# Kernel tuning notes

Hardware: AMD Instinct MI355X
Metric: run time of the kernel (lower is better)

Reference implementation:

```python
import jax, jax.numpy as jnp
import numpy as np

SIZE = 512
ATTN = 64      # per-head attention_size
OUT = 64       # per-head output_size
HEADS = 8

def setup_inputs() -> dict:
    key = jax.random.key(0)
    ks = jax.random.split(key, 7)
    s = 0.02
    return {
        "x":  jax.random.normal(ks[0], (4, 2048, SIZE), dtype=jnp.float32),
        "Wq": jax.random.normal(ks[1], (SIZE, ATTN * HEADS), dtype=jnp.float32) * s,
        "bq": jax.random.normal(ks[2], (ATTN * HEADS,), dtype=jnp.float32) * s,
        "Wk": jax.random.normal(ks[3], (SIZE, ATTN), dtype=jnp.float32) * s,  # shared key, no bias
        "Wv": jax.random.normal(ks[4], (SIZE, OUT * HEADS), dtype=jnp.float32) * s,
        "bv": jax.random.normal(ks[5], (OUT * HEADS,), dtype=jnp.float32) * s,
    }

def reference(x, Wq, bq, Wk, Wv, bv):
    B, S, _ = x.shape
    q = (x @ Wq + bq).reshape(B, S, HEADS, ATTN)   # (B,S,H,A)
    k = x @ Wk                                      # (B,S,A) shared across heads
    v = (x @ Wv + bv).reshape(B, S, HEADS, OUT)     # (B,S,H,O)
    # NOTE: original divides by sqrt(seq_len), not sqrt(head_dim)
    scale = 1.0 / np.sqrt(S).astype(np.float32)
    scores = jnp.einsum("bqha,bka->bhqk", q, k) * scale  # (B,H,S,S)
    causal = jnp.tril(jnp.ones((S, S), dtype=bool))
    scores = jnp.where(causal, scores, -jnp.inf)
    attn = jax.nn.softmax(scores, axis=-1)
    out = jnp.einsum("bhqk,bkho->bqho", attn, v)    # (B,S,H,O)
    return out.reshape(B, S, HEADS * OUT)
```

## Files before the change

kernel.cpp:

```cpp
#include <hip/hip_runtime.h>
#include <math.h>


typedef _Float16 half8 __attribute__((ext_vector_type(8)));
typedef _Float16 half4 __attribute__((ext_vector_type(4)));
typedef float float4v __attribute__((ext_vector_type(4)));
typedef unsigned int u32;

#define SCL2E 0.031885926f

__device__ inline float4v mfma16(half8 a, half8 b, float4v c) {
    return __builtin_amdgcn_mfma_f32_16x16x32_f16(a, b, c, 0, 0, 0);
}
__device__ inline void load16(const _Float16* g, _Float16* l) {
    __builtin_amdgcn_global_load_lds((const __attribute__((address_space(1))) u32*)g,
                                     (__attribute__((address_space(3))) u32*)l, 16, 0, 0);
}

__global__ __launch_bounds__(256) void prep(
    const float* __restrict__ x, const float* __restrict__ Wq,
    const float* __restrict__ Wk, const float* __restrict__ Wv,
    _Float16* __restrict__ xh, _Float16* __restrict__ wqt,
    _Float16* __restrict__ wkt, _Float16* __restrict__ wvt) {
    const int bid = blockIdx.x;
    if (bid < 2048) {
        size_t base = (size_t)bid * 2048 + (size_t)threadIdx.x * 8;
        const float4* xp = (const float4*)(x + base);
        float4 f0 = xp[0], f1 = xp[1];
        half8 h = {(_Float16)f0.x, (_Float16)f0.y, (_Float16)f0.z, (_Float16)f0.w,
                   (_Float16)f1.x, (_Float16)f1.y, (_Float16)f1.z, (_Float16)f1.w};
        *(half8*)(xh + base) = h;
    } else {
        int r = bid - 2048;
        const float* W; _Float16* WT; int N, bx, by;
        if (r < 256)      { W = Wq; WT = wqt; N = 512; bx = r & 15; by = r >> 4; }
        else if (r < 288) { r -= 256; W = Wk; WT = wkt; N = 64;  bx = r & 1;  by = r >> 1; }
        else              { r -= 288; W = Wv; WT = wvt; N = 512; bx = r & 15; by = r >> 4; }
        __shared__ float T[32][33];
        const int tx = threadIdx.x & 31, ty = threadIdx.x >> 5;
        const int n0 = bx * 32, k0 = by * 32;
#pragma unroll
        for (int i = 0; i < 4; ++i)
            T[ty + 8 * i][tx] = W[(size_t)(k0 + ty + 8 * i) * N + n0 + tx];
        __syncthreads();
#pragma unroll
        for (int i = 0; i < 4; ++i)
            WT[(size_t)(n0 + ty + 8 * i) * 512 + k0 + tx] = (_Float16)T[tx][ty + 8 * i];
    }
}

__global__ __launch_bounds__(256) void qkv_gemm(
    const _Float16* __restrict__ xh,
    const _Float16* __restrict__ wqt, const _Float16* __restrict__ wkt,
    const _Float16* __restrict__ wvt,
    const float* __restrict__ bq, const float* __restrict__ bv,
    _Float16* __restrict__ q_ws, _Float16* __restrict__ kt_ws, _Float16* __restrict__ vt_ws) {
    __shared__ __align__(16) _Float16 Xs[2][8192];
    __shared__ __align__(16) _Float16 Ws[2][4096];

    const int m0 = blockIdx.x * 128;
    const int nt = blockIdx.y;
    const _Float16* WT;
    const float* bias;
    if (nt < 8)       { WT = wqt + (size_t)nt * 64 * 512; bias = bq + nt * 64; }
    else if (nt == 8) { WT = wkt;                          bias = nullptr; }
    else              { WT = wvt + (size_t)(nt - 9) * 64 * 512; bias = bv + (nt - 9) * 64; }

    const int tid = threadIdx.x;
    const int w = tid >> 6, lane = tid & 63, quad = lane >> 4, cl = lane & 15;
    const int lrow = lane >> 3;
    const int lgc = (lane & 7) ^ lrow;
    const _Float16* xg = xh + (size_t)(m0 + lrow) * 512 + lgc * 8;
    const _Float16* wg = WT + (size_t)lrow * 512 + lgc * 8;

    const int g0 = (quad ^ (cl & 7)) << 3;
    const int g1 = ((quad ^ 4) ^ (cl & 7)) << 3;

    float4v acc[2][4] = {};

#pragma unroll
    for (int c = 0; c < 4; ++c) {
        int cc = w * 4 + c;
        load16(xg + (size_t)cc * 8 * 512, Xs[0] + cc * 512);
    }
#pragma unroll
    for (int c = 0; c < 2; ++c) {
        int cc = w * 2 + c;
        load16(wg + (size_t)cc * 8 * 512, Ws[0] + cc * 512);
    }

    for (int ki = 0; ki < 8; ++ki) {
        const int cb = ki & 1, nb = cb ^ 1;
        __syncthreads();
        if (ki < 7) {
            const int kk = (ki + 1) * 64;
#pragma unroll
            for (int c = 0; c < 4; ++c) {
                int cc = w * 4 + c;
                load16(xg + (size_t)cc * 8 * 512 + kk, Xs[nb] + cc * 512);
            }
#pragma unroll
            for (int c = 0; c < 2; ++c) {
                int cc = w * 2 + c;
                load16(wg + (size_t)cc * 8 * 512 + kk, Ws[nb] + cc * 512);
            }
        }
#pragma unroll
        for (int c = 0; c < 2; ++c) {
            const int g = c ? g1 : g0;
#pragma unroll
            for (int s = 0; s < 2; ++s) {
                half8 a = *(const half8*)(Xs[cb] + (w * 32 + s * 16 + cl) * 64 + g);
#pragma unroll
                for (int j = 0; j < 4; ++j) {
                    half8 b = *(const half8*)(Ws[cb] + (j * 16 + cl) * 64 + g);
                    acc[s][j] = mfma16(a, b, acc[s][j]);
                }
            }
        }
    }

    if (nt < 8) {
#pragma unroll
        for (int s = 0; s < 2; ++s)
#pragma unroll
            for (int j = 0; j < 4; ++j)
#pragma unroll
                for (int r = 0; r < 4; ++r) {
                    int lr = w * 32 + s * 16 + quad * 4 + r;
                    int col = j * 16 + cl;
                    q_ws[(size_t)(m0 + lr) * 512 + nt * 64 + col] =
                        (_Float16)((acc[s][j][r] + bias[col]) * SCL2E);
                }
    } else if (nt == 8) {
#pragma unroll
        for (int s = 0; s < 2; ++s)
#pragma unroll
            for (int j = 0; j < 4; ++j)
#pragma unroll
                for (int r = 0; r < 4; ++r) {
                    int grow = m0 + w * 32 + s * 16 + quad * 4 + r;
                    int b = grow >> 11, t = (grow >> 6) & 31, row = grow & 63;
                    int col = j * 16 + cl;
                    kt_ws[((size_t)(b * 32 + t) << 12) + row * 64 +
                          (((col >> 3) ^ (row & 7)) << 3) + (col & 7)] = (_Float16)acc[s][j][r];
                }
    } else {
        const int h = nt - 9;
#pragma unroll
        for (int s = 0; s < 2; ++s)
#pragma unroll
            for (int j = 0; j < 4; ++j)
#pragma unroll
                for (int r = 0; r < 4; ++r) {
                    int grow = m0 + w * 32 + s * 16 + quad * 4 + r;
                    int b = grow >> 11, t = (grow >> 6) & 31, row = grow & 63;
                    int o = j * 16 + cl;
                    int kap = ((row & 15) << 2) + (row >> 4);
                    vt_ws[(((size_t)(b * 8 + h) * 32 + t) << 12) + o * 64 +
                          (((kap >> 3) ^ (o & 7)) << 3) + (kap & 7)] =
                        (_Float16)(acc[s][j][r] + bias[o]);
                }
    }
}

__global__ __launch_bounds__(512, 2) void attn(
    const _Float16* __restrict__ q_ws, const _Float16* __restrict__ kt_ws,
    const _Float16* __restrict__ vt_ws, float* __restrict__ out) {
    __shared__ __align__(16) _Float16 Ks[2][2][4096];
    __shared__ __align__(16) _Float16 VTs[2][2][4096];
    __shared__ __align__(16) _Float16 Ps[8][1024];

    const int bh = blockIdx.x, b = bh >> 3, h = bh & 7;
    const int p = 31 - blockIdx.y;
    const int q0 = p * 64;
    const int nmax = (p + 2) >> 1;

    const int bS = b * 2048;
    const int tid = threadIdx.x;
    const int w = tid >> 6, lane = tid & 63, quad = lane >> 4, cl = lane & 15;
    const int g = w >> 2, wl = w & 3;
    const int tbase = g ? nmax : 0;
    const int nit = g ? (p + 1 - nmax) : nmax;

    const _Float16* kbase = kt_ws + ((size_t)(b * 32) << 12);
    const _Float16* vbase = vt_ws + ((size_t)((b * 8 + h) * 32) << 12);

    const int g0 = (quad ^ (cl & 7)) << 3;
    const int g1 = ((quad ^ 4) ^ (cl & 7)) << 3;
    const int so0 = wl * 1024 + lane * 8;

    const _Float16* qbase = q_ws + (size_t)(bS + q0 + wl * 16 + cl) * 512 + h * 64;
    half8 qa0 = *(const half8*)(qbase + quad * 8);
    half8 qa1 = *(const half8*)(qbase + 32 + quad * 8);

    float4v oacc[4] = {};
    float l_run[4] = {0.f, 0.f, 0.f, 0.f};

    if (nit > 0) {
        const _Float16* kt = kbase + ((size_t)tbase << 12);
        const _Float16* vt = vbase + ((size_t)tbase << 12);
        load16(kt + so0,       &Ks[g][0][wl * 1024]);
        load16(kt + so0 + 512, &Ks[g][0][wl * 1024 + 512]);
        load16(vt + so0,       &VTs[g][0][wl * 1024]);
        load16(vt + so0 + 512, &VTs[g][0][wl * 1024 + 512]);
    }

    for (int t = 0; t < nmax; ++t) {
        const int cb = t & 1, nb = cb ^ 1;
        __syncthreads();
        const int tg = tbase + t;
        if (t + 1 < nit) {
            const _Float16* kt = kbase + ((size_t)(tg + 1) << 12);
            const _Float16* vt = vbase + ((size_t)(tg + 1) << 12);
            load16(kt + so0,       &Ks[g][nb][wl * 1024]);
            load16(kt + so0 + 512, &Ks[g][nb][wl * 1024 + 512]);
            load16(vt + so0,       &VTs[g][nb][wl * 1024]);
            load16(vt + so0 + 512, &VTs[g][nb][wl * 1024 + 512]);
        }
        if (t < nit) {
            if (tg != p) {
                float4v sfr[4];
#pragma unroll
                for (int j = 0; j < 4; ++j) {
                    const _Float16* kr = &Ks[g][cb][(j * 16 + cl) * 64];
                    half8 b0 = *(const half8*)(kr + g0);
                    half8 b1 = *(const half8*)(kr + g1);
                    float4v a_ = {0.f, 0.f, 0.f, 0.f};
                    a_ = mfma16(qa0, b0, a_);
                    a_ = mfma16(qa1, b1, a_);
                    sfr[j] = a_;
                }
#pragma unroll
                for (int r = 0; r < 4; ++r) {
                    float p0 = exp2f(sfr[0][r]), p1 = exp2f(sfr[1][r]);
                    float p2 = exp2f(sfr[2][r]), p3 = exp2f(sfr[3][r]);
                    l_run[r] += (p0 + p1) + (p2 + p3);
                    int rr = quad * 4 + r;
                    half4 ph = {(_Float16)p0, (_Float16)p1, (_Float16)p2, (_Float16)p3};
                    *(half4*)&Ps[w][rr * 64 + ((((cl >> 1) ^ (rr & 7)) << 3) | ((cl & 1) << 2))] = ph;
                }
            } else {
                const int jmax = wl;
                float4v sfr[4];
#pragma unroll
                for (int j = 0; j < 4; ++j) {
                    if (j <= jmax) {
                        const _Float16* kr = &Ks[g][cb][(j * 16 + cl) * 64];
                        half8 b0 = *(const half8*)(kr + g0);
                        half8 b1 = *(const half8*)(kr + g1);
                        float4v a_ = {0.f, 0.f, 0.f, 0.f};
                        a_ = mfma16(qa0, b0, a_);
                        a_ = mfma16(qa1, b1, a_);
                        sfr[j] = a_;
                    }
                }
#pragma unroll
                for (int r = 0; r < 4; ++r) {
                    float pj[4];
#pragma unroll
                    for (int j = 0; j < 4; ++j) {
                        bool live = (j < jmax) || (j == jmax && cl <= quad * 4 + r);
                        pj[j] = live ? exp2f(sfr[j][r]) : 0.f;
                    }
                    l_run[r] += (pj[0] + pj[1]) + (pj[2] + pj[3]);
                    int rr = quad * 4 + r;
                    half4 ph = {(_Float16)pj[0], (_Float16)pj[1], (_Float16)pj[2], (_Float16)pj[3]};
                    *(half4*)&Ps[w][rr * 64 + ((((cl >> 1) ^ (rr & 7)) << 3) | ((cl & 1) << 2))] = ph;
                }
            }
            const _Float16* PB = &Ps[w][cl * 64];
            half8 pa0 = *(const half8*)(PB + g0);
            half8 pa1 = *(const half8*)(PB + g1);
#pragma unroll
            for (int jo = 0; jo < 4; ++jo) {
                const _Float16* vr = &VTs[g][cb][(jo * 16 + cl) * 64];
                half8 v0 = *(const half8*)(vr + g0);
                half8 v1 = *(const half8*)(vr + g1);
                oacc[jo] = mfma16(pa0, v0, oacc[jo]);
                oacc[jo] = mfma16(pa1, v1, oacc[jo]);
            }
        }
    }

    __syncthreads();
    float* Obuf = (float*)&Ks[1][0][0];
    float* Lbuf = (float*)&Ps[4][0];
    if (g == 1) {
#pragma unroll
        for (int jo = 0; jo < 4; ++jo)
#pragma unroll
            for (int r = 0; r < 4; ++r) {
                int row = wl * 16 + quad * 4 + r;
                Obuf[row * 64 + jo * 16 + cl] = oacc[jo][r];
            }
#pragma unroll
        for (int r = 0; r < 4; ++r) {
            int row = wl * 16 + quad * 4 + r;
            Lbuf[row * 16 + cl] = l_run[r];
        }
    }
    __syncthreads();
    if (g == 0) {
#pragma unroll
        for (int r = 0; r < 4; ++r) {
            int row = wl * 16 + quad * 4 + r;
            float l = l_run[r] + Lbuf[row * 16 + cl];
            l += __shfl_xor(l, 1);
            l += __shfl_xor(l, 2);
            l += __shfl_xor(l, 4);
            l += __shfl_xor(l, 8);
            float inv = 1.0f / l;
            float* op = out + (size_t)(bS + q0 + row) * 512 + h * 64 + cl;
            op[0]  = (oacc[0][r] + Obuf[row * 64 +      cl]) * inv;
            op[16] = (oacc[1][r] + Obuf[row * 64 + 16 + cl]) * inv;
            op[32] = (oacc[2][r] + Obuf[row * 64 + 32 + cl]) * inv;
            op[48] = (oacc[3][r] + Obuf[row * 64 + 48 + cl]) * inv;
        }
    }
}

extern "C" void kernel_launch(void* const* d_in, const int* in_sizes, int n_in,
                              void* d_out, int out_size, void* d_ws, size_t ws_size,
                              hipStream_t stream) {
    const float* x  = (const float*)d_in[0];
    const float* Wq = (const float*)d_in[1];
    const float* bq = (const float*)d_in[2];
    const float* Wk = (const float*)d_in[3];
    const float* Wv = (const float*)d_in[4];
    const float* bv = (const float*)d_in[5];
    float* out = (float*)d_out;

    char* ws = (char*)d_ws;
    _Float16* q_ws  = (_Float16*)(ws);
    _Float16* kt_ws = (_Float16*)(ws + 8388608);
    _Float16* vt_ws = (_Float16*)(ws + 9437184);
    _Float16* wqt   = (_Float16*)(ws + 17825792);
    _Float16* wkt   = (_Float16*)(ws + 18350080);
    _Float16* wvt   = (_Float16*)(ws + 18415616);
    _Float16* xh    = (_Float16*)(ws + 18939904);

    prep<<<dim3(2592), dim3(256), 0, stream>>>(x, Wq, Wk, Wv, xh, wqt, wkt, wvt);

    qkv_gemm<<<dim3(64, 17), dim3(256), 0, stream>>>(
        xh, wqt, wkt, wvt, bq, bv, q_ws, kt_ws, vt_ws);

    attn<<<dim3(32, 32), dim3(512), 0, stream>>>(q_ws, kt_ws, vt_ws, out);
}
```

Baseline: 142.8 us.

## Skew group-1 warps to overlap P·V of previous tile with next QK

Refactors the tile loop into staging, QK/softmax and PV lambdas. The second warp group now runs a skewed software pipeline: it does the P·V of the previous tile, then stages the next K tile and the current V tile, then computes QK for the current tile, with a final P·V after the loop. The goal is to stagger the MFMA and LDS phases between the two warp groups and hide load latency. The V for the current tile is loaded within the same iteration without a barrier before its use, and the Lbuf location moves, so there are correctness and timing risks around sync and async LDS loads.

Result: faster. 137.9 us (median of 3 runs) (-3.4%).

```diff
diff --git a/kernel.cpp b/kernel.cpp
--- a/kernel.cpp
+++ b/kernel.cpp
@@ -197,33 +197,49 @@
     float4v oacc[4] = {};
     float l_run[4] = {0.f, 0.f, 0.f, 0.f};
 
-    if (nit > 0) {
-        const _Float16* kt = kbase + ((size_t)tbase << 12);
-        const _Float16* vt = vbase + ((size_t)tbase << 12);
-        load16(kt + so0,       &Ks[g][0][wl * 1024]);
-        load16(kt + so0 + 512, &Ks[g][0][wl * 1024 + 512]);
-        load16(vt + so0,       &VTs[g][0][wl * 1024]);
-        load16(vt + so0 + 512, &VTs[g][0][wl * 1024 + 512]);
-    }
-
-    for (int t = 0; t < nmax; ++t) {
-        const int cb = t & 1, nb = cb ^ 1;
-        __syncthreads();
-        const int tg = tbase + t;
-        if (t + 1 < nit) {
-            const _Float16* kt = kbase + ((size_t)(tg + 1) << 12);
-            const _Float16* vt = vbase + ((size_t)(tg + 1) << 12);
-            load16(kt + so0,       &Ks[g][nb][wl * 1024]);
-            load16(kt + so0 + 512, &Ks[g][nb][wl * 1024 + 512]);
-            load16(vt + so0,       &VTs[g][nb][wl * 1024]);
-            load16(vt + so0 + 512, &VTs[g][nb][wl * 1024 + 512]);
-        }
-        if (t < nit) {
-            if (tg != p) {
-                float4v sfr[4];
-#pragma unroll
-                for (int j = 0; j < 4; ++j) {
-                    const _Float16* kr = &Ks[g][cb][(j * 16 + cl) * 64];
+    _Float16* KsG = &Ks[g][0][0];
+    _Float16* VsG = &VTs[g][0][0];
+
+    auto stageK = [&](int tile, int buf) {
+        const _Float16* kt = kbase + ((size_t)tile << 12);
+        load16(kt + so0,       KsG + buf * 4096 + wl * 1024);
+        load16(kt + so0 + 512, KsG + buf * 4096 + wl * 1024 + 512);
+    };
+    auto stageV = [&](int tile, int buf) {
+        const _Float16* vt = vbase + ((size_t)tile << 12);
+        load16(vt + so0,       VsG + buf * 4096 + wl * 1024);
+        load16(vt + so0 + 512, VsG + buf * 4096 + wl * 1024 + 512);
+    };
+    auto qk_sm = [&](int tg, int buf) {
+        const _Float16* KB = KsG + buf * 4096;
+        if (tg != p) {
+            float4v sfr[4];
+#pragma unroll
+            for (int j = 0; j < 4; ++j) {
+                const _Float16* kr = KB + (j * 16 + cl) * 64;
+                half8 b0 = *(const half8*)(kr + g0);
+                half8 b1 = *(const half8*)(kr + g1);
+                float4v a_ = {0.f, 0.f, 0.f, 0.f};
+                a_ = mfma16(qa0, b0, a_);
+                a_ = mfma16(qa1, b1, a_);
+                sfr[j] = a_;
+            }
+#pragma unroll
+            for (int r = 0; r < 4; ++r) {
+                float p0 = exp2f(sfr[0][r]), p1 = exp2f(sfr[1][r]);
+                float p2 = exp2f(sfr[2][r]), p3 = exp2f(sfr[3][r]);
+                l_run[r] += (p0 + p1) + (p2 + p3);
+                int rr = quad * 4 + r;
+                half4 ph = {(_Float16)p0, (_Float16)p1, (_Float16)p2, (_Float16)p3};
+                *(half4*)&Ps[w][rr * 64 + ((((cl >> 1) ^ (rr & 7)) << 3) | ((cl & 1) << 2))] = ph;
+            }
+        } else {
+            const int jmax = wl;
+            float4v sfr[4];
+#pragma unroll
+            for (int j = 0; j < 4; ++j) {
+                if (j <= jmax) {
+                    const _Float16* kr = KB + (j * 16 + cl) * 64;
                     half8 b0 = *(const half8*)(kr + g0);
                     half8 b1 = *(const half8*)(kr + g1);
                     float4v a_ = {0.f, 0.f, 0.f, 0.f};
@@ -231,61 +247,65 @@
                     a_ = mfma16(qa1, b1, a_);
                     sfr[j] = a_;
                 }
-#pragma unroll
-                for (int r = 0; r < 4; ++r) {
-                    float p0 = exp2f(sfr[0][r]), p1 = exp2f(sfr[1][r]);
-                    float p2 = exp2f(sfr[2][r]), p3 = exp2f(sfr[3][r]);
-                    l_run[r] += (p0 + p1) + (p2 + p3);
-                    int rr = quad * 4 + r;
-                    half4 ph = {(_Float16)p0, (_Float16)p1, (_Float16)p2, (_Float16)p3};
-                    *(half4*)&Ps[w][rr * 64 + ((((cl >> 1) ^ (rr & 7)) << 3) | ((cl & 1) << 2))] = ph;
-                }
-            } else {
-                const int jmax = wl;
-                float4v sfr[4];
+            }
+#pragma unroll
+            for (int r = 0; r < 4; ++r) {
+                float pj[4];
 #pragma unroll
                 for (int j = 0; j < 4; ++j) {
-                    if (j <= jmax) {
-                        const _Float16* kr = &Ks[g][cb][(j * 16 + cl) * 64];
-                        half8 b0 = *(const half8*)(kr + g0);
-                        half8 b1 = *(const half8*)(kr + g1);
-                        float4v a_ = {0.f, 0.f, 0.f, 0.f};
-                        a_ = mfma16(qa0, b0, a_);
-                        a_ = mfma16(qa1, b1, a_);
-                        sfr[j] = a_;
-                    }
-                }
-#pragma unroll
-                for (int r = 0; r < 4; ++r) {
-                    float pj[4];
-#pragma unroll
-                    for (int j = 0; j < 4; ++j) {
-                        bool live = (j < jmax) || (j == jmax && cl <= quad * 4 + r);
-                        pj[j] = live ? exp2f(sfr[j][r]) : 0.f;
-                    }
-                    l_run[r] += (pj[0] + pj[1]) + (pj[2] + pj[3]);
-                    int rr = quad * 4 + r;
-                    half4 ph = {(_Float16)pj[0], (_Float16)pj[1], (_Float16)pj[2], (_Float16)pj[3]};
-                    *(half4*)&Ps[w][rr * 64 + ((((cl >> 1) ^ (rr & 7)) << 3) | ((cl & 1) << 2))] = ph;
-                }
-            }
-            const _Float16* PB = &Ps[w][cl * 64];
-            half8 pa0 = *(const half8*)(PB + g0);
-            half8 pa1 = *(const half8*)(PB + g1);
-#pragma unroll
-            for (int jo = 0; jo < 4; ++jo) {
-                const _Float16* vr = &VTs[g][cb][(jo * 16 + cl) * 64];
-                half8 v0 = *(const half8*)(vr + g0);
-                half8 v1 = *(const half8*)(vr + g1);
-                oacc[jo] = mfma16(pa0, v0, oacc[jo]);
-                oacc[jo] = mfma16(pa1, v1, oacc[jo]);
+                    bool live = (j < jmax) || (j == jmax && cl <= quad * 4 + r);
+                    pj[j] = live ? exp2f(sfr[j][r]) : 0.f;
+                }
+                l_run[r] += (pj[0] + pj[1]) + (pj[2] + pj[3]);
+                int rr = quad * 4 + r;
+                half4 ph = {(_Float16)pj[0], (_Float16)pj[1], (_Float16)pj[2], (_Float16)pj[3]};
+                *(half4*)&Ps[w][rr * 64 + ((((cl >> 1) ^ (rr & 7)) << 3) | ((cl & 1) << 2))] = ph;
+            }
+        }
+    };
+    auto pv = [&](int buf) {
+        const _Float16* PB = &Ps[w][cl * 64];
+        half8 pa0 = *(const half8*)(PB + g0);
+        half8 pa1 = *(const half8*)(PB + g1);
+        const _Float16* VB = VsG + buf * 4096;
+#pragma unroll
+        for (int jo = 0; jo < 4; ++jo) {
+            const _Float16* vr = VB + (jo * 16 + cl) * 64;
+            half8 v0 = *(const half8*)(vr + g0);
+            half8 v1 = *(const half8*)(vr + g1);
+            oacc[jo] = mfma16(pa0, v0, oacc[jo]);
+            oacc[jo] = mfma16(pa1, v1, oacc[jo]);
+        }
+    };
+
+    if (nit > 0) {
+        stageK(tbase, 0);
+        if (g == 0) stageV(tbase, 0);
+    }
+
+    for (int t = 0; t < nmax; ++t) {
+        const int cb = t & 1, nb = cb ^ 1;
+        __syncthreads();
+        const int tg = tbase + t;
+        if (g == 0) {
+            if (t + 1 < nit) { stageK(tg + 1, nb); stageV(tg + 1, nb); }
+            qk_sm(tg, cb);
+            pv(cb);
+        } else {
+            if (t > 0 && t - 1 < nit) pv(nb);
+            if (t + 1 < nit) stageK(tg + 1, nb);
+            if (t < nit) {
+                stageV(tg, cb);
+                qk_sm(tg, cb);
             }
         }
     }
 
     __syncthreads();
+    if (g == 1 && nit == nmax) pv((nmax - 1) & 1);
+
     float* Obuf = (float*)&Ks[1][0][0];
-    float* Lbuf = (float*)&Ps[4][0];
+    float* Lbuf = (float*)&VTs[0][0][0];
     if (g == 1) {
 #pragma unroll
         for (int jo = 0; jo < 4; ++jo)
```
